# Optimization experiments

Hardware: AMD Instinct MI355X
Metric: run time of the kernel (lower is better)

## Reference

```python
import jax, jax.numpy as jnp
import numpy as np
import math

ROPE_BASE = 10000.0

def _rope(x):
    # x: [B, H, S, D]; interleaved-pair LLaMA-style rotary embedding
    S, D = x.shape[-2], x.shape[-1]
    inv_freq = 1.0 / (ROPE_BASE ** (jnp.arange(0, D, 2, dtype=jnp.float32) / D))  # [D/2]
    ang = jnp.arange(S, dtype=jnp.float32)[:, None] * inv_freq[None, :]           # [S, D/2]
    cos, sin = jnp.cos(ang), jnp.sin(ang)
    x1, x2 = x[..., 0::2], x[..., 1::2]
    r1 = x1 * cos - x2 * sin
    r2 = x1 * sin + x2 * cos
    return jnp.stack([r1, r2], axis=-1).reshape(x.shape)

def setup_inputs() -> dict:
    key = jax.random.key(0)
    ks = jax.random.split(key, 5)
    B, S, E = 2, 2048, 2048
    scale = 1.0 / math.sqrt(E)
    return {
        "x": jax.random.normal(ks[0], (B, S, E), dtype=jnp.float32),
        "Wq": jax.random.normal(ks[1], (E, E), dtype=jnp.float32) * scale,
        "Wk": jax.random.normal(ks[2], (E, E), dtype=jnp.float32) * scale,
        "Wv": jax.random.normal(ks[3], (E, E), dtype=jnp.float32) * scale,
        "Wo": jax.random.normal(ks[4], (E, E), dtype=jnp.float32) * scale,
    }

def reference(x, Wq, Wk, Wv, Wo):
    B, S, E = x.shape
    H = 16
    D = E // H
    # projections (torch Linear: y = x @ W^T, weights stored [out, in])
    def proj(W):
        y = jnp.einsum('bse,oe->bso', x, W)
        return y.reshape(B, S, H, D).transpose(0, 2, 1, 3)  # [B,H,S,D]
    q, k, v = proj(Wq), proj(Wk), proj(Wv)
    q_rot, k_rot = _rope(q), _rope(k)
    scores = jnp.einsum('bhqd,bhkd->bhqk', q_rot, k_rot) / jnp.sqrt(jnp.float32(D))
    causal = jnp.tril(jnp.ones((S, S), dtype=bool))
    scores = jnp.where(causal[None, None], scores, -jnp.inf)
    attn = jax.nn.softmax(scores, axis=-1)
    out = jnp.einsum('bhqk,bhkd->bhqd', attn, v)
    out = out.transpose(0, 2, 1, 3).reshape(B, S, E)
    attn_out = jnp.einsum('bse,oe->bso', out, Wo)
    return (attn_out, k, v)
```

## Files before the change

kernel.cpp:

```cpp
#include <hip/hip_runtime.h>

typedef __attribute__((ext_vector_type(8))) short short8;
typedef __attribute__((ext_vector_type(4))) float floatx4;

#define B_ 2
#define S_ 2048
#define E_ 2048
#define H_ 16
#define D_ 128

#define NEG_S  (-3.0e4f)
#define LOG2E  1.4426950408889634f

__device__ inline float bf2f(unsigned short u) {
    union { unsigned int i; float f; } v; v.i = ((unsigned int)u) << 16; return v.f;
}
__device__ inline unsigned short f2bf(float f) {
    union { float f; unsigned int i; } v; v.f = f;
    unsigned int r = v.i + 0x7FFFu + ((v.i >> 16) & 1u);
    return (unsigned short)(r >> 16);
}

__device__ inline void gload_lds16(const void* g, void* l) {
    __builtin_amdgcn_global_load_lds((__attribute__((address_space(1))) void*)(void*)g,
                                     (__attribute__((address_space(3))) void*)l, 16, 0, 0);
}

__global__ void rope_tab(float* __restrict__ cosT, float* __restrict__ sinT) {
    int idx = blockIdx.x * 256 + threadIdx.x;
    int s = idx >> 6, j = idx & 63;
    float inv = exp2f(-(float)(2 * j) * (13.287712379549449f / 128.0f));
    float ang = (float)s * inv;
    cosT[idx] = cosf(ang);
    sinT[idx] = sinf(ang);
}

__global__ __launch_bounds__(256) void cvt_bf16(const float* __restrict__ in,
                                                unsigned short* __restrict__ out, int n8) {
    int i = blockIdx.x * 256 + threadIdx.x;
    if (i >= n8) return;
    float4 f0 = *(const float4*)(in + (size_t)i * 8);
    float4 f1 = *(const float4*)(in + (size_t)i * 8 + 4);
    unsigned short u[8] = {f2bf(f0.x), f2bf(f0.y), f2bf(f0.z), f2bf(f0.w),
                           f2bf(f1.x), f2bf(f1.y), f2bf(f1.z), f2bf(f1.w)};
    *(uint4*)(out + (size_t)i * 8) = *(uint4*)u;
}

__global__ __launch_bounds__(256) void prep_k(const float* __restrict__ K,
                                              unsigned short* __restrict__ Kr,
                                              const float* __restrict__ cosT,
                                              const float* __restrict__ sinT) {
    int idx = blockIdx.x * 256 + threadIdx.x;
    int g = idx & 15;
    int s = (idx >> 4) & (S_ - 1);
    const float* src = K + (size_t)idx * 8;
    float4 f0 = *(const float4*)src;
    float4 f1 = *(const float4*)(src + 4);
    float xs[8] = {f0.x, f0.y, f0.z, f0.w, f1.x, f1.y, f1.z, f1.w};
    unsigned short u[8];
    int jb = g * 4;
#pragma unroll
    for (int i = 0; i < 4; i++) {
        float c = cosT[s * 64 + jb + i], sn = sinT[s * 64 + jb + i];
        float x1 = xs[2 * i], x2 = xs[2 * i + 1];
        u[2 * i]     = f2bf(x1 * c - x2 * sn);
        u[2 * i + 1] = f2bf(x1 * sn + x2 * c);
    }
    *(uint4*)(Kr + (size_t)idx * 8) = *(uint4*)u;
}

__global__ __launch_bounds__(256) void prep_v(const float* __restrict__ V,
                                              unsigned short* __restrict__ Vt) {
    __shared__ unsigned short Ls[64][130];
    int bh = blockIdx.y;
    int s0 = blockIdx.x * 64;
    int t = threadIdx.x;
    const float* src = V + ((size_t)bh * S_ + s0) * D_;
#pragma unroll
    for (int it = 0; it < 4; it++) {
        int r = it * 16 + (t >> 4), d0 = (t & 15) * 8;
        float4 f0 = *(const float4*)&src[(size_t)r * D_ + d0];
        float4 f1 = *(const float4*)&src[(size_t)r * D_ + d0 + 4];
        unsigned short u[8] = {f2bf(f0.x), f2bf(f0.y), f2bf(f0.z), f2bf(f0.w),
                               f2bf(f1.x), f2bf(f1.y), f2bf(f1.z), f2bf(f1.w)};
#pragma unroll
        for (int i = 0; i < 8; i++) Ls[r][d0 + i] = u[i];
    }
    __syncthreads();
    unsigned short* dst = Vt + (size_t)bh * D_ * S_;
#pragma unroll
    for (int it = 0; it < 4; it++) {
        int d = it * 32 + (t >> 3), ss = (t & 7) * 8;
        unsigned short u[8];
#pragma unroll
        for (int i = 0; i < 8; i++) u[i] = Ls[ss + i][d];
        *(uint4*)&dst[(size_t)d * S_ + s0 + ss] = *(uint4*)u;
    }
}

__global__ __launch_bounds__(256) void gemm128(const unsigned short* __restrict__ A,
                                               const unsigned short* __restrict__ Bw,
                                               void* __restrict__ dst, int dstMode) {
    __shared__ __align__(16) unsigned short As[128][32];
    __shared__ __align__(16) unsigned short Bs[128][32];
    int t = threadIdx.x;
    int wave = t >> 6, lane = t & 63;
    int quad = lane >> 4, l16 = lane & 15;
    int wr = wave >> 1, wc = wave & 1;

    floatx4 acc[4][4];
#pragma unroll
    for (int m = 0; m < 4; m++)
#pragma unroll
        for (int n = 0; n < 4; n++) acc[m][n] = (floatx4)(0.f);

    int srow = lane >> 2;
    int sg = lane & 3;
    const size_t aRow0 = (size_t)blockIdx.x * 128;
    const size_t bRow0 = (size_t)blockIdx.y * 128;

    for (int k0 = 0; k0 < E_; k0 += 32) {
#pragma unroll
        for (int i = 0; i < 2; i++) {
            int lr = wave * 32 + i * 16 + srow;
            int gg = sg ^ ((lr >> 1) & 3);
            gload_lds16(A + (aRow0 + lr) * E_ + k0 + gg * 8, &As[wave * 32 + i * 16][0]);
            gload_lds16(Bw + (bRow0 + lr) * E_ + k0 + gg * 8, &Bs[wave * 32 + i * 16][0]);
        }
        __syncthreads();
        short8 af[4], bfr[4];
#pragma unroll
        for (int m = 0; m < 4; m++) {
            int r = wr * 64 + m * 16 + l16;
            af[m] = *(const short8*)((const char*)As + r * 64 + ((quad ^ ((r >> 1) & 3)) << 4));
        }
#pragma unroll
        for (int n = 0; n < 4; n++) {
            int r = wc * 64 + n * 16 + l16;
            bfr[n] = *(const short8*)((const char*)Bs + r * 64 + ((quad ^ ((r >> 1) & 3)) << 4));
        }
#pragma unroll
        for (int m = 0; m < 4; m++)
#pragma unroll
            for (int n = 0; n < 4; n++)
                acc[m][n] = __builtin_amdgcn_mfma_f32_16x16x32_bf16(af[m], bfr[n], acc[m][n], 0, 0, 0);
        __syncthreads();
    }
#pragma unroll
    for (int m = 0; m < 4; m++)
#pragma unroll
        for (int n = 0; n < 4; n++)
#pragma unroll
            for (int rr = 0; rr < 4; rr++) {
                int mg = (int)aRow0 + wr * 64 + m * 16 + quad * 4 + rr;
                int ng = (int)bRow0 + wc * 64 + n * 16 + l16;
                float val = acc[m][n][rr];
                if (dstMode == 0) {
                    ((float*)dst)[(size_t)mg * E_ + ng] = val;
                } else if (dstMode == 1) {
                    int b = mg >> 11, s = mg & 2047, h = ng >> 7, d = ng & 127;
                    ((float*)dst)[(((size_t)(b * H_ + h)) * S_ + s) * D_ + d] = val;
                } else {
                    ((unsigned short*)dst)[(size_t)mg * E_ + ng] = f2bf(val);
                }
            }
}

__global__ __launch_bounds__(256) void attn_fast6(const unsigned short* __restrict__ Qf,
                                                  const unsigned short* __restrict__ Kr,
                                                  const unsigned short* __restrict__ Vt,
                                                  const float* __restrict__ cosT,
                                                  const float* __restrict__ sinT,
                                                  unsigned short* __restrict__ Omid) {
    __shared__ __align__(16) unsigned short Ks[64][128];
    __shared__ __align__(16) unsigned short Vs[128][64];
    __shared__ __align__(16) unsigned short Ps[4][16][64];

    int t = threadIdx.x;
    int wave = t >> 6, lane = t & 63;
    int quad = lane >> 4, l16 = lane & 15;
    int orig = blockIdx.x;
    int L = (orig & 7) * 64 + (orig >> 3);
    int h = L >> 5;
    int q5 = L & 31;
    int qtile = (h & 1) ? (31 - q5) : q5;
    int b = blockIdx.y;

    const unsigned short* Qb = Qf + (size_t)b * S_ * E_;
    const unsigned short* Kh = Kr + ((size_t)(b * H_ + h)) * S_ * D_;
    const unsigned short* Vh = Vt + ((size_t)(b * H_ + h)) * D_ * S_;

    int sq = qtile * 64 + wave * 16 + l16;
    short8 qf[4];
#pragma unroll
    for (int ks = 0; ks < 4; ks++) {
        int d0 = ks * 32 + quad * 8;
        union { uint4 u4; unsigned short u[8]; } un;
        un.u4 = *(const uint4*)&Qb[(size_t)sq * E_ + h * D_ + d0];
#pragma unroll
        for (int i = 0; i < 4; i++) {
            int j = (d0 >> 1) + i;
            float c = cosT[sq * 64 + j], s = sinT[sq * 64 + j];
            float x1 = bf2f(un.u[2 * i]), x2 = bf2f(un.u[2 * i + 1]);
            un.u[2 * i] = f2bf(x1 * c - x2 * s);
            un.u[2 * i + 1] = f2bf(x1 * s + x2 * c);
        }
        qf[ks] = *(short8*)un.u;
    }

    floatx4 O[8];
#pragma unroll
    for (int i = 0; i < 8; i++) O[i] = (floatx4)(0.f);
    float mrow[4], lrow[4];
#pragma unroll
    for (int r = 0; r < 4; r++) { mrow[r] = NEG_S; lrow[r] = 0.f; }

    const float scale = 0.08838834764831845f;
    char* pbase = (char*)&Ps[wave][0][0];

    for (int kt = 0; kt <= qtile; kt++) {
#pragma unroll
        for (int i = 0; i < 4; i++) {
            int r = wave * 16 + i * 4 + (lane >> 4);
            int g = (lane & 15) ^ (r & 7);
            gload_lds16(&Kh[(size_t)(kt * 64 + r) * D_ + g * 8], &Ks[wave * 16 + i * 4][0]);
        }
#pragma unroll
        for (int i = 0; i < 4; i++) {
            int r = wave * 32 + i * 8 + (lane >> 3);
            int g = (lane & 7) ^ (r & 7);
            gload_lds16(&Vh[(size_t)r * S_ + kt * 64 + g * 8], &Vs[wave * 32 + i * 8][0]);
        }
        __syncthreads();

        floatx4 sc[4];
#pragma unroll
        for (int ct = 0; ct < 4; ct++) sc[ct] = (floatx4)(0.f);
        __builtin_amdgcn_s_setprio(1);
#pragma unroll
        for (int ks = 0; ks < 4; ks++) {
#pragma unroll
            for (int ct = 0; ct < 4; ct++) {
                int r = ct * 16 + l16;
                short8 kf = *(const short8*)((const char*)Ks + r * 256 +
                                             ((((ks << 2) + quad) ^ (r & 7)) << 4));
                sc[ct] = __builtin_amdgcn_mfma_f32_16x16x32_bf16(qf[ks], kf, sc[ct], 0, 0, 0);
            }
        }
        __builtin_amdgcn_s_setprio(0);
        int rowbase = qtile * 64 + wave * 16 + quad * 4;
#pragma unroll
        for (int ct = 0; ct < 4; ct++) {
            int col = kt * 64 + ct * 16 + l16;
#pragma unroll
            for (int rr = 0; rr < 4; rr++) {
                float x = sc[ct][rr] * scale;
                sc[ct][rr] = (col > rowbase + rr) ? NEG_S : x;
            }
        }
        float alpha[4];
#pragma unroll
        for (int rr = 0; rr < 4; rr++) {
            float mx = fmaxf(fmaxf(sc[0][rr], sc[1][rr]), fmaxf(sc[2][rr], sc[3][rr]));
            mx = fmaxf(mx, __shfl_xor(mx, 1));
            mx = fmaxf(mx, __shfl_xor(mx, 2));
            mx = fmaxf(mx, __shfl_xor(mx, 4));
            mx = fmaxf(mx, __shfl_xor(mx, 8));
            float mnew = fmaxf(mrow[rr], mx);
            alpha[rr] = exp2f((mrow[rr] - mnew) * LOG2E);
            mrow[rr] = mnew;
        }
#pragma unroll
        for (int rr = 0; rr < 4; rr++) {
            float ps = 0.f;
#pragma unroll
            for (int ct = 0; ct < 4; ct++) {
                float p = exp2f((sc[ct][rr] - mrow[rr]) * LOG2E);
                sc[ct][rr] = p;
                ps += p;
            }
            ps += __shfl_xor(ps, 1);
            ps += __shfl_xor(ps, 2);
            ps += __shfl_xor(ps, 4);
            ps += __shfl_xor(ps, 8);
            lrow[rr] = lrow[rr] * alpha[rr] + ps;
        }
#pragma unroll
        for (int c8 = 0; c8 < 8; c8++)
#pragma unroll
            for (int rr = 0; rr < 4; rr++) O[c8][rr] *= alpha[rr];

#pragma unroll
        for (int ct = 0; ct < 4; ct++)
#pragma unroll
            for (int rr = 0; rr < 4; rr++) {
                int row = quad * 4 + rr;
                int byteoff = (row << 7) + (((ct * 16 + l16) << 1) ^ ((row & 7) << 4));
                *(unsigned short*)(pbase + byteoff) = f2bf(sc[ct][rr]);
            }
        asm volatile("s_waitcnt lgkmcnt(0)" ::: "memory");
        __builtin_amdgcn_sched_barrier(0);

        __builtin_amdgcn_s_setprio(1);
#pragma unroll
        for (int ka2 = 0; ka2 < 2; ka2++) {
            int pboff = (l16 << 7) + ((ka2 * 64 + quad * 16) ^ ((l16 & 7) << 4));
            short8 pa = *(const short8*)(pbase + pboff);
#pragma unroll
            for (int c8 = 0; c8 < 8; c8++) {
                int r = c8 * 16 + l16;
                short8 vf = *(const short8*)((const char*)Vs + r * 128 +
                                             ((((ka2 << 2) + quad) ^ (r & 7)) << 4));
                O[c8] = __builtin_amdgcn_mfma_f32_16x16x32_bf16(pa, vf, O[c8], 0, 0, 0);
            }
        }
        __builtin_amdgcn_s_setprio(0);
        asm volatile("s_waitcnt lgkmcnt(0)" ::: "memory");
        __builtin_amdgcn_sched_barrier(0);
        __syncthreads();
    }

#pragma unroll
    for (int rr = 0; rr < 4; rr++) {
        float inv = 1.f / lrow[rr];
        int row = qtile * 64 + wave * 16 + quad * 4 + rr;
#pragma unroll
        for (int c8 = 0; c8 < 8; c8++) {
            int d = c8 * 16 + l16;
            Omid[((size_t)b * S_ + row) * E_ + h * D_ + d] = f2bf(O[c8][rr] * inv);
        }
    }
}


__global__ __launch_bounds__(256) void gemm_bt(const void* __restrict__ A,
                                               const float* __restrict__ Bw,
                                               void* __restrict__ dst,
                                               int aBf16, int dstMode) {
    __shared__ __align__(16) unsigned short As[64][40];
    __shared__ __align__(16) unsigned short Bs[64][40];
    int t = threadIdx.x;
    int wave = t >> 6, lane = t & 63;
    int quad = lane >> 4, l16 = lane & 15;
    floatx4 acc[4];
#pragma unroll
    for (int i = 0; i < 4; i++) acc[i] = (floatx4)(0.f);

    int r = t >> 2, kc = (t & 3) * 8;
    int ra = blockIdx.x * 64 + r;
    int rb = blockIdx.y * 64 + r;

    for (int k0 = 0; k0 < E_; k0 += 32) {
        if (aBf16) {
            const unsigned short* Ab = (const unsigned short*)A + (size_t)ra * E_ + kc + k0;
            *(uint4*)&As[r][kc] = *(const uint4*)Ab;
        } else {
            const float* Af = (const float*)A + (size_t)ra * E_ + kc + k0;
            float4 f0 = *(const float4*)Af;
            float4 f1 = *(const float4*)(Af + 4);
            unsigned short u[8] = {f2bf(f0.x), f2bf(f0.y), f2bf(f0.z), f2bf(f0.w),
                                   f2bf(f1.x), f2bf(f1.y), f2bf(f1.z), f2bf(f1.w)};
            *(uint4*)&As[r][kc] = *(uint4*)u;
        }
        {
            const float* Bf = Bw + (size_t)rb * E_ + kc + k0;
            float4 g0 = *(const float4*)Bf;
            float4 g1 = *(const float4*)(Bf + 4);
            unsigned short u[8] = {f2bf(g0.x), f2bf(g0.y), f2bf(g0.z), f2bf(g0.w),
                                   f2bf(g1.x), f2bf(g1.y), f2bf(g1.z), f2bf(g1.w)};
            *(uint4*)&Bs[r][kc] = *(uint4*)u;
        }
        __syncthreads();
        short8 a = *(const short8*)&As[wave * 16 + l16][quad * 8];
#pragma unroll
        for (int ct = 0; ct < 4; ct++) {
            short8 bfr = *(const short8*)&Bs[ct * 16 + l16][quad * 8];
            acc[ct] = __builtin_amdgcn_mfma_f32_16x16x32_bf16(a, bfr, acc[ct], 0, 0, 0);
        }
        __syncthreads();
    }
#pragma unroll
    for (int ct = 0; ct < 4; ct++) {
#pragma unroll
        for (int rr = 0; rr < 4; rr++) {
            int m = blockIdx.x * 64 + wave * 16 + quad * 4 + rr;
            int n = blockIdx.y * 64 + ct * 16 + l16;
            float val = acc[ct][rr];
            if (dstMode == 0) {
                ((float*)dst)[(size_t)m * E_ + n] = val;
            } else if (dstMode == 1) {
                int b = m >> 11, s = m & 2047, h = n >> 7, d = n & 127;
                ((float*)dst)[(((size_t)(b * H_ + h)) * S_ + s) * D_ + d] = val;
            } else {
                ((unsigned short*)dst)[(size_t)m * E_ + n] = f2bf(val);
            }
        }
    }
}

__global__ __launch_bounds__(256) void attn_fwd(const unsigned short* __restrict__ Qf,
                                                const float* __restrict__ Kb0,
                                                const float* __restrict__ Vb0,
                                                const float* __restrict__ cosT,
                                                const float* __restrict__ sinT,
                                                unsigned short* __restrict__ Omid,
                                                int qtile0) {
    __shared__ __align__(16) unsigned short Ks[64][136];
    __shared__ __align__(16) unsigned short Vt[128][72];
    __shared__ __align__(16) unsigned short Ps[4][16][72];

    int t = threadIdx.x;
    int wave = t >> 6, lane = t & 63;
    int quad = lane >> 4, l16 = lane & 15;
    int qtile = qtile0 + blockIdx.x, h = blockIdx.y;
    const float* Kb = Kb0 + (size_t)h * S_ * D_;
    const float* Vb = Vb0 + (size_t)h * S_ * D_;

    int sq = qtile * 64 + wave * 16 + l16;
    short8 qf[4];
#pragma unroll
    for (int ks = 0; ks < 4; ks++) {
        int d0 = ks * 32 + quad * 8;
        union { uint4 u4; unsigned short u[8]; } un;
        un.u4 = *(const uint4*)&Qf[(size_t)sq * E_ + h * D_ + d0];
#pragma unroll
        for (int i = 0; i < 4; i++) {
            int j = (d0 >> 1) + i;
            float c = cosT[sq * 64 + j], s = sinT[sq * 64 + j];
            float x1 = bf2f(un.u[2 * i]), x2 = bf2f(un.u[2 * i + 1]);
            un.u[2 * i] = f2bf(x1 * c - x2 * s);
            un.u[2 * i + 1] = f2bf(x1 * s + x2 * c);
        }
        qf[ks] = *(short8*)un.u;
    }

    floatx4 O[8];
#pragma unroll
    for (int i = 0; i < 8; i++) O[i] = (floatx4)(0.f);
    float mrow[4], lrow[4];
#pragma unroll
    for (int r = 0; r < 4; r++) { mrow[r] = NEG_S; lrow[r] = 0.f; }

    const float scale = 0.08838834764831845f;

    for (int kt = 0; kt <= qtile; kt++) {
        __syncthreads();
        int r = t >> 2;
#pragma unroll
        for (int it = 0; it < 4; it++) {
            int d0 = (t & 3) * 8 + it * 32;
            int sk = kt * 64 + r;
            float4 ka = *(const float4*)&Kb[(size_t)sk * D_ + d0];
            float4 kb2 = *(const float4*)&Kb[(size_t)sk * D_ + d0 + 4];
            float xs[8] = {ka.x, ka.y, ka.z, ka.w, kb2.x, kb2.y, kb2.z, kb2.w};
            unsigned short u[8];
#pragma unroll
            for (int i = 0; i < 4; i++) {
                int j = (d0 >> 1) + i;
                float c = cosT[sk * 64 + j], s = sinT[sk * 64 + j];
                float x1 = xs[2 * i], x2 = xs[2 * i + 1];
                u[2 * i]     = f2bf(x1 * c - x2 * s);
                u[2 * i + 1] = f2bf(x1 * s + x2 * c);
            }
            *(uint4*)&Ks[r][d0] = *(uint4*)u;
            float4 va = *(const float4*)&Vb[(size_t)sk * D_ + d0];
            float4 vb2 = *(const float4*)&Vb[(size_t)sk * D_ + d0 + 4];
            float vs[8] = {va.x, va.y, va.z, va.w, vb2.x, vb2.y, vb2.z, vb2.w};
#pragma unroll
            for (int i = 0; i < 8; i++) Vt[d0 + i][r] = f2bf(vs[i]);
        }
        __syncthreads();

        floatx4 sc[4];
#pragma unroll
        for (int ct = 0; ct < 4; ct++) sc[ct] = (floatx4)(0.f);
#pragma unroll
        for (int ks = 0; ks < 4; ks++) {
#pragma unroll
            for (int ct = 0; ct < 4; ct++) {
                short8 kf = *(const short8*)&Ks[ct * 16 + l16][ks * 32 + quad * 8];
                sc[ct] = __builtin_amdgcn_mfma_f32_16x16x32_bf16(qf[ks], kf, sc[ct], 0, 0, 0);
            }
        }
        int rowbase = qtile * 64 + wave * 16 + quad * 4;
#pragma unroll
        for (int ct = 0; ct < 4; ct++) {
            int col = kt * 64 + ct * 16 + l16;
#pragma unroll
            for (int rr = 0; rr < 4; rr++) {
                float x = sc[ct][rr] * scale;
                sc[ct][rr] = (col > rowbase + rr) ? NEG_S : x;
            }
        }
        float alpha[4];
#pragma unroll
        for (int rr = 0; rr < 4; rr++) {
            float mx = fmaxf(fmaxf(sc[0][rr], sc[1][rr]), fmaxf(sc[2][rr], sc[3][rr]));
            mx = fmaxf(mx, __shfl_xor(mx, 1));
            mx = fmaxf(mx, __shfl_xor(mx, 2));
            mx = fmaxf(mx, __shfl_xor(mx, 4));
            mx = fmaxf(mx, __shfl_xor(mx, 8));
            float mnew = fmaxf(mrow[rr], mx);
            alpha[rr] = exp2f((mrow[rr] - mnew) * LOG2E);
            mrow[rr] = mnew;
        }
#pragma unroll
        for (int rr = 0; rr < 4; rr++) {
            float ps = 0.f;
#pragma unroll
            for (int ct = 0; ct < 4; ct++) {
                float p = exp2f((sc[ct][rr] - mrow[rr]) * LOG2E);
                sc[ct][rr] = p;
                ps += p;
            }
            ps += __shfl_xor(ps, 1);
            ps += __shfl_xor(ps, 2);
            ps += __shfl_xor(ps, 4);
            ps += __shfl_xor(ps, 8);
            lrow[rr] = lrow[rr] * alpha[rr] + ps;
        }
#pragma unroll
        for (int c8 = 0; c8 < 8; c8++)
#pragma unroll
            for (int rr = 0; rr < 4; rr++) O[c8][rr] *= alpha[rr];

#pragma unroll
        for (int ct = 0; ct < 4; ct++)
#pragma unroll
            for (int rr = 0; rr < 4; rr++)
                Ps[wave][quad * 4 + rr][ct * 16 + l16] = f2bf(sc[ct][rr]);
        __syncthreads();

#pragma unroll
        for (int ka2 = 0; ka2 < 2; ka2++) {
            short8 pa = *(const short8*)&Ps[wave][l16][ka2 * 32 + quad * 8];
#pragma unroll
            for (int c8 = 0; c8 < 8; c8++) {
                short8 vf = *(const short8*)&Vt[c8 * 16 + l16][ka2 * 32 + quad * 8];
                O[c8] = __builtin_amdgcn_mfma_f32_16x16x32_bf16(pa, vf, O[c8], 0, 0, 0);
            }
        }
    }

#pragma unroll
    for (int rr = 0; rr < 4; rr++) {
        float inv = 1.f / lrow[rr];
        int lrw = blockIdx.x * 64 + wave * 16 + quad * 4 + rr;
#pragma unroll
        for (int c8 = 0; c8 < 8; c8++) {
            int d = c8 * 16 + l16;
            Omid[(size_t)lrw * E_ + h * D_ + d] = f2bf(O[c8][rr] * inv);
        }
    }
}

extern "C" void kernel_launch(void* const* d_in, const int* in_sizes, int n_in,
                              void* d_out, int out_size, void* d_ws, size_t ws_size,
                              hipStream_t stream) {
    const float* x  = (const float*)d_in[0];
    const float* Wq = (const float*)d_in[1];
    const float* Wk = (const float*)d_in[2];
    const float* Wv = (const float*)d_in[3];
    const float* Wo = (const float*)d_in[4];

    float* out_attn = (float*)d_out;
    float* out_k = out_attn + (size_t)B_ * H_ * S_ * D_;
    float* out_v = out_k + (size_t)B_ * H_ * S_ * D_;

    char* ws = (char*)d_ws;
    float* cosT = (float*)ws;
    float* sinT = cosT + S_ * (D_ / 2);
    size_t tab_bytes = 2u * S_ * (D_ / 2) * sizeof(float);

    size_t krBytes  = (size_t)B_ * H_ * S_ * D_ * 2;
    size_t wbBytes  = (size_t)E_ * E_ * 2;
    size_t midBytes = (size_t)B_ * S_ * E_ * 2;
    size_t needFast = tab_bytes + 2 * krBytes + wbBytes + midBytes;

    hipLaunchKernelGGL(rope_tab, dim3(512), dim3(256), 0, stream, cosT, sinT);

    if (ws_size >= needFast) {
        unsigned short* Kr  = (unsigned short*)(ws + tab_bytes);
        unsigned short* Vt  = Kr + (size_t)B_ * H_ * S_ * D_;
        unsigned short* Wb  = Vt + (size_t)B_ * H_ * S_ * D_;
        unsigned short* mid = Wb + (size_t)E_ * E_;
        unsigned short* xb    = (unsigned short*)out_attn;
        unsigned short* q_tmp = (unsigned short*)(out_attn + (size_t)S_ * E_);

        hipLaunchKernelGGL(cvt_bf16, dim3(4096), dim3(256), 0, stream, x, xb, 1048576);

        hipLaunchKernelGGL(cvt_bf16, dim3(2048), dim3(256), 0, stream, Wq, Wb, 524288);
        hipLaunchKernelGGL(gemm128, dim3(32, 16), dim3(256), 0, stream, xb, Wb, (void*)q_tmp, 3);

        hipLaunchKernelGGL(cvt_bf16, dim3(2048), dim3(256), 0, stream, Wk, Wb, 524288);
        hipLaunchKernelGGL(gemm128, dim3(32, 16), dim3(256), 0, stream, xb, Wb, (void*)out_k, 1);
        hipLaunchKernelGGL(prep_k, dim3(4096), dim3(256), 0, stream, out_k, Kr, cosT, sinT);

        hipLaunchKernelGGL(cvt_bf16, dim3(2048), dim3(256), 0, stream, Wv, Wb, 524288);
        hipLaunchKernelGGL(gemm128, dim3(32, 16), dim3(256), 0, stream, xb, Wb, (void*)out_v, 1);
        hipLaunchKernelGGL(prep_v, dim3(32, 32), dim3(256), 0, stream, out_v, Vt);

        hipLaunchKernelGGL(cvt_bf16, dim3(2048), dim3(256), 0, stream, Wo, Wb, 524288);

        hipLaunchKernelGGL(attn_fast6, dim3(512, B_), dim3(256), 0, stream,
                           q_tmp, Kr, Vt, cosT, sinT, mid);
        hipLaunchKernelGGL(gemm128, dim3(32, 16), dim3(256), 0, stream, mid, Wb,
                           (void*)out_attn, 0);
    } else {
        unsigned short* q_tmp = (unsigned short*)(out_attn + (size_t)S_ * E_);
        unsigned short* mid = (unsigned short*)(ws + tab_bytes);
        size_t avail = ws_size > tab_bytes ? ws_size - tab_bytes : 0;
        int R = 64;
        for (int r = 2048; r >= 64; r >>= 1) {
            if ((size_t)r * E_ * 2 <= avail) { R = r; break; }
        }

        dim3 gg(64, 32);
        hipLaunchKernelGGL(gemm_bt, gg, dim3(256), 0, stream, (const void*)x, Wq, (void*)q_tmp, 0, 3);
        hipLaunchKernelGGL(gemm_bt, gg, dim3(256), 0, stream, (const void*)x, Wk, (void*)out_k, 0, 1);
        hipLaunchKernelGGL(gemm_bt, gg, dim3(256), 0, stream, (const void*)x, Wv, (void*)out_v, 0, 1);

        const size_t bhsd = (size_t)H_ * S_ * D_;
        for (int b = 0; b < B_; b++) {
            const unsigned short* qb = q_tmp + (size_t)b * S_ * E_;
            for (int c = 0; c < S_ / 64; c += R / 64) {
                hipLaunchKernelGGL(attn_fwd, dim3(R / 64, H_), dim3(256), 0, stream,
                                   qb, out_k + b * bhsd, out_v + b * bhsd,
                                   cosT, sinT, mid, c);
                hipLaunchKernelGGL(gemm_bt, dim3(R / 64, 32), dim3(256), 0, stream,
                                   (const void*)mid, Wo,
                                   (void*)(out_attn + ((size_t)b * S_ + c * 64) * E_), 1, 0);
            }
        }
    }
}
```

Before: 534.0 us.

## Double-buffer GEMM LDS tiles with K=64 stages and prefetch next stage

The projection GEMM now stages 64-wide K tiles into two LDS buffers and issues the global-to-LDS loads for the next tile before computing on the current one. This overlaps memory latency with MFMA work and halves the number of barriers per K sweep. The swizzle moves to an 8-group XOR pattern, and s_setprio raises wave priority during the MFMA section. LDS use per block grows fourfold, to 64 KB, which may reduce occupancy.

```diff
diff --git a/kernel.cpp b/kernel.cpp
--- a/kernel.cpp
+++ b/kernel.cpp
@@ -101,8 +101,8 @@
 __global__ __launch_bounds__(256) void gemm128(const unsigned short* __restrict__ A,
                                                const unsigned short* __restrict__ Bw,
                                                void* __restrict__ dst, int dstMode) {
-    __shared__ __align__(16) unsigned short As[128][32];
-    __shared__ __align__(16) unsigned short Bs[128][32];
+    __shared__ __align__(16) unsigned short As[2][128][64];
+    __shared__ __align__(16) unsigned short Bs[2][128][64];
     int t = threadIdx.x;
     int wave = t >> 6, lane = t & 63;
     int quad = lane >> 4, l16 = lane & 15;
@@ -114,38 +114,56 @@
 #pragma unroll
         for (int n = 0; n < 4; n++) acc[m][n] = (floatx4)(0.f);
 
-    int srow = lane >> 2;
-    int sg = lane & 3;
     const size_t aRow0 = (size_t)blockIdx.x * 128;
     const size_t bRow0 = (size_t)blockIdx.y * 128;
 
-    for (int k0 = 0; k0 < E_; k0 += 32) {
-#pragma unroll
-        for (int i = 0; i < 2; i++) {
-            int lr = wave * 32 + i * 16 + srow;
-            int gg = sg ^ ((lr >> 1) & 3);
-            gload_lds16(A + (aRow0 + lr) * E_ + k0 + gg * 8, &As[wave * 32 + i * 16][0]);
-            gload_lds16(Bw + (bRow0 + lr) * E_ + k0 + gg * 8, &Bs[wave * 32 + i * 16][0]);
-        }
-        __syncthreads();
-        short8 af[4], bfr[4];
-#pragma unroll
-        for (int m = 0; m < 4; m++) {
-            int r = wr * 64 + m * 16 + l16;
-            af[m] = *(const short8*)((const char*)As + r * 64 + ((quad ^ ((r >> 1) & 3)) << 4));
-        }
-#pragma unroll
-        for (int n = 0; n < 4; n++) {
-            int r = wc * 64 + n * 16 + l16;
-            bfr[n] = *(const short8*)((const char*)Bs + r * 64 + ((quad ^ ((r >> 1) & 3)) << 4));
-        }
-#pragma unroll
-        for (int m = 0; m < 4; m++)
-#pragma unroll
-            for (int n = 0; n < 4; n++)
-                acc[m][n] = __builtin_amdgcn_mfma_f32_16x16x32_bf16(af[m], bfr[n], acc[m][n], 0, 0, 0);
-        __syncthreads();
-    }
+#define GSTAGE(BUF, K0)                                                          \
+    {                                                                            \
+        _Pragma("unroll")                                                        \
+        for (int i_ = 0; i_ < 4; i_++) {                                         \
+            int r_ = wave * 32 + i_ * 8 + (lane >> 3);                           \
+            int g_ = (lane & 7) ^ (r_ & 7);                                      \
+            gload_lds16(A + (aRow0 + r_) * E_ + (K0) + g_ * 8,                   \
+                        &As[BUF][wave * 32 + i_ * 8][0]);                        \
+            gload_lds16(Bw + (bRow0 + r_) * E_ + (K0) + g_ * 8,                  \
+                        &Bs[BUF][wave * 32 + i_ * 8][0]);                        \
+        }                                                                        \
+    }
+
+    GSTAGE(0, 0);
+    __syncthreads();
+
+    for (int it = 0; it < E_ / 64; it++) {
+        int cur = it & 1;
+        if (it + 1 < E_ / 64) GSTAGE(cur ^ 1, (it + 1) * 64);
+
+        __builtin_amdgcn_s_setprio(1);
+#pragma unroll
+        for (int ks = 0; ks < 2; ks++) {
+            short8 af[4], bfr[4];
+#pragma unroll
+            for (int m = 0; m < 4; m++) {
+                int r = wr * 64 + m * 16 + l16;
+                af[m] = *(const short8*)((const char*)&As[cur][0][0] + r * 128 +
+                                         ((((ks << 2) + quad) ^ (r & 7)) << 4));
+            }
+#pragma unroll
+            for (int n = 0; n < 4; n++) {
+                int r = wc * 64 + n * 16 + l16;
+                bfr[n] = *(const short8*)((const char*)&Bs[cur][0][0] + r * 128 +
+                                          ((((ks << 2) + quad) ^ (r & 7)) << 4));
+            }
+#pragma unroll
+            for (int m = 0; m < 4; m++)
+#pragma unroll
+                for (int n = 0; n < 4; n++)
+                    acc[m][n] = __builtin_amdgcn_mfma_f32_16x16x32_bf16(af[m], bfr[n], acc[m][n], 0, 0, 0);
+        }
+        __builtin_amdgcn_s_setprio(0);
+        __syncthreads();
+    }
+#undef GSTAGE
+
 #pragma unroll
     for (int m = 0; m < 4; m++)
 #pragma unroll
```

Result: faster. 487.9 us (-8.6%).
